# Performance work log

Measured on AMD Instinct MI355X. Metric: run time of the kernel, lower is better.

Reference implementation:

```python
import jax, jax.numpy as jnp
import numpy as np
import math

B, NQ, NK = 32, 1024, 1024
DQ = DK = DV = 512
H = 8
EPS = 1e-5


def _layernorm(x, g, b):
    mu = jnp.mean(x, axis=-1, keepdims=True)
    var = jnp.mean(jnp.square(x - mu), axis=-1, keepdims=True)
    return (x - mu) * jax.lax.rsqrt(var + EPS) * g + b


def setup_inputs() -> dict:
    key = jax.random.key(0)
    ks = jax.random.split(key, 8)
    s = 0.03  # small init scale for linear weights
    return {
        "Q": jax.random.normal(ks[0], (B, NQ, DQ), jnp.float32),
        "K": jax.random.normal(ks[1], (B, NK, DK), jnp.float32),
        "Wq": jax.random.normal(ks[2], (DQ, DV), jnp.float32) * s,
        "bq": jnp.zeros((DV,), jnp.float32),
        "Wk": jax.random.normal(ks[3], (DK, DV), jnp.float32) * s,
        "bk": jnp.zeros((DV,), jnp.float32),
        "Wv": jax.random.normal(ks[4], (DK, DV), jnp.float32) * s,
        "bv": jnp.zeros((DV,), jnp.float32),
        "Wo": jax.random.normal(ks[5], (DV, DV), jnp.float32) * s,
        "bo": jnp.zeros((DV,), jnp.float32),
        "g0": jnp.ones((DV,), jnp.float32),
        "beta0": jnp.zeros((DV,), jnp.float32),
        "g1": jnp.ones((DV,), jnp.float32),
        "beta1": jnp.zeros((DV,), jnp.float32),
    }


def reference(Q, K, Wq, bq, Wk, bk, Wv, bv, Wo, bo, g0, beta0, g1, beta1):
    b, nq, _ = Q.shape
    nk = K.shape[1]
    d = DV // H  # head dim (dim_split)

    q = Q @ Wq + bq            # [B, Nq, DV]
    k = K @ Wk + bk            # [B, Nk, DV]
    v = K @ Wv + bv            # [B, Nk, DV]

    # torch.cat(x.split(d, 2), 0) == reshape to [B,N,H,d] then stack heads on batch dim
    qh = q.reshape(b, nq, H, d).transpose(2, 0, 1, 3)  # [H, B, Nq, d]
    kh = k.reshape(b, nk, H, d).transpose(2, 0, 1, 3)  # [H, B, Nk, d]
    vh = v.reshape(b, nk, H, d).transpose(2, 0, 1, 3)  # [H, B, Nk, d]

    # NOTE: scaled by sqrt(dim_V), and softmax over the QUERY axis (torch dim=1)
    scores = jnp.einsum('hbqd,hbkd->hbqk', qh, kh) / math.sqrt(DV)
    A = jax.nn.softmax(scores, axis=2)                 # over Nq (faithful to source)
    oh = qh + jnp.einsum('hbqk,hbkd->hbqd', A, vh)     # residual on Q_

    out = oh.transpose(1, 2, 0, 3).reshape(b, nq, DV)  # merge heads back
    out = _layernorm(out, g0, beta0)
    out = out + jax.nn.relu(out @ Wo + bo)
    out = _layernorm(out, g1, beta1)
    return out
```

## Files before the change

kernel.cpp:

```cpp
#include <hip/hip_runtime.h>

#define Bz  32
#define NQz 1024
#define NKz 1024
#define SCALE 0.04419417382415922f

typedef __bf16 bf16_t;
typedef bf16_t bf16x8 __attribute__((ext_vector_type(8)));
typedef bf16_t bf16x4 __attribute__((ext_vector_type(4)));
typedef float  f32x4  __attribute__((ext_vector_type(4)));

#define MFMA16(a, b, c) __builtin_amdgcn_mfma_f32_16x16x32_bf16(a, b, c, 0, 0, 0)

__device__ __forceinline__ void gll16(const void* g, void* l) {
  __builtin_amdgcn_global_load_lds(
      (const __attribute__((address_space(1))) void*)g,
      (__attribute__((address_space(3))) void*)l, 16, 0, 0);
}

__device__ __forceinline__ bf16x8 cvt8(float4 a, float4 b) {
  bf16x8 r;
  r[0] = (bf16_t)a.x; r[1] = (bf16_t)a.y; r[2] = (bf16_t)a.z; r[3] = (bf16_t)a.w;
  r[4] = (bf16_t)b.x; r[5] = (bf16_t)b.y; r[6] = (bf16_t)b.z; r[7] = (bf16_t)b.w;
  return r;
}

__global__ void transpose_w(const float* __restrict__ W0, const float* __restrict__ W1,
                            const float* __restrict__ W2, const float* __restrict__ W3,
                            bf16_t* __restrict__ out) {
  __shared__ float tile[32][33];
  const float* W = blockIdx.z == 0 ? W0 : blockIdx.z == 1 ? W1 : blockIdx.z == 2 ? W2 : W3;
  bf16_t* o = out + (size_t)blockIdx.z * 512 * 512;
  const int n0 = blockIdx.x * 32, k0 = blockIdx.y * 32;
  const int tx = threadIdx.x, ty = threadIdx.y;
  for (int i = 0; i < 4; i++)
    tile[ty + i * 8][tx] = W[(size_t)(k0 + ty + i * 8) * 512 + n0 + tx];
  __syncthreads();
  for (int i = 0; i < 4; i++)
    o[(size_t)(n0 + ty + i * 8) * 512 + k0 + tx] = (bf16_t)tile[tx][ty + i * 8];
}

template <int DUAL>
__global__ __launch_bounds__(256) void gemm_f32a(const float* __restrict__ A,
                                                 const bf16_t* __restrict__ Wt,
                                                 const float* __restrict__ b0v,
                                                 const float* __restrict__ b1v,
                                                 float mult0,
                                                 bf16_t* __restrict__ C0,
                                                 bf16_t* __restrict__ C1) {
  __shared__ __align__(16) bf16_t As[128][40];
  __shared__ __align__(16) bf16_t Bs[128 * 32];
  const int t = threadIdx.x;
  const int wave = t >> 6, lane = t & 63;
  const int quad = lane >> 4, l16 = lane & 15;
  const int wm = wave & 1, wn = wave >> 1;
  const int m0 = blockIdx.x * 128, n0 = blockIdx.y * 128;
  const int r = t >> 1, half = t & 1;
  const int drow = lane >> 2;
  const int dg = (lane & 3) ^ ((lane >> 3) & 3);

  f32x4 acc[4][4] = {};

  for (int k0 = 0; k0 < 512; k0 += 32) {
    __syncthreads();
    for (int p = 0; p < 2; p++) {
      const bf16_t* src = Wt + (size_t)(n0 + p * 64 + wave * 16 + drow) * 512 + k0 + dg * 8;
      gll16(src, &Bs[(p * 256 + wave * 64) * 8]);
    }
    {
      const float* ap = A + (size_t)(m0 + r) * 512 + k0 + half * 16;
      float4 a0 = *(const float4*)(ap + 0);
      float4 a1 = *(const float4*)(ap + 4);
      float4 a2 = *(const float4*)(ap + 8);
      float4 a3 = *(const float4*)(ap + 12);
      *(bf16x8*)&As[r][half * 16 + 0] = cvt8(a0, a1);
      *(bf16x8*)&As[r][half * 16 + 8] = cvt8(a2, a3);
    }
    __syncthreads();
    bf16x8 af[4], bfv[4];
    for (int mt = 0; mt < 4; mt++)
      af[mt] = *(const bf16x8*)&As[wm * 64 + mt * 16 + l16][quad * 8];
    for (int nt = 0; nt < 4; nt++) {
      const int rB = wn * 64 + nt * 16 + l16;
      bfv[nt] = *(const bf16x8*)&Bs[rB * 32 + ((quad ^ ((rB >> 1) & 3)) * 8)];
    }
    for (int mt = 0; mt < 4; mt++)
      for (int nt = 0; nt < 4; nt++)
        acc[mt][nt] = MFMA16(af[mt], bfv[nt], acc[mt][nt]);
  }

  const float* bias = (!DUAL || n0 < 512) ? b0v : b1v;
  bf16_t* C = (!DUAL || n0 < 512) ? C0 : C1;
  const float mult = (!DUAL || n0 < 512) ? mult0 : 1.0f;
  const int nb = (!DUAL || n0 < 512) ? n0 : n0 - 512;
  for (int mt = 0; mt < 4; mt++) {
    for (int nt = 0; nt < 4; nt++) {
      const int row = m0 + wm * 64 + mt * 16 + quad * 4;
      const int col = nb + wn * 64 + nt * 16 + l16;
      const float bv = bias[col];
      for (int rg = 0; rg < 4; rg++)
        C[(size_t)(row + rg) * 512 + col] = (bf16_t)((acc[mt][nt][rg] + bv) * mult);
    }
  }
}

__global__ __launch_bounds__(256) void gemm_bf16a(const bf16_t* __restrict__ A,
                                                  const bf16_t* __restrict__ Wt,
                                                  const float* __restrict__ bias,
                                                  bf16_t* __restrict__ C) {
  __shared__ __align__(16) bf16_t As[128][40];
  __shared__ __align__(16) bf16_t Bs[128 * 32];
  const int t = threadIdx.x;
  const int wave = t >> 6, lane = t & 63;
  const int quad = lane >> 4, l16 = lane & 15;
  const int wm = wave & 1, wn = wave >> 1;
  const int m0 = blockIdx.x * 128, n0 = blockIdx.y * 128;
  const int r = t >> 1, half = t & 1;
  const int drow = lane >> 2;
  const int dg = (lane & 3) ^ ((lane >> 3) & 3);

  f32x4 acc[4][4] = {};

  for (int k0 = 0; k0 < 512; k0 += 32) {
    __syncthreads();
    for (int p = 0; p < 2; p++) {
      const bf16_t* src = Wt + (size_t)(n0 + p * 64 + wave * 16 + drow) * 512 + k0 + dg * 8;
      gll16(src, &Bs[(p * 256 + wave * 64) * 8]);
    }
    {
      const bf16_t* ap = A + (size_t)(m0 + r) * 512 + k0 + half * 16;
      *(bf16x8*)&As[r][half * 16 + 0] = *(const bf16x8*)(ap + 0);
      *(bf16x8*)&As[r][half * 16 + 8] = *(const bf16x8*)(ap + 8);
    }
    __syncthreads();
    bf16x8 af[4], bfv[4];
    for (int mt = 0; mt < 4; mt++)
      af[mt] = *(const bf16x8*)&As[wm * 64 + mt * 16 + l16][quad * 8];
    for (int nt = 0; nt < 4; nt++) {
      const int rB = wn * 64 + nt * 16 + l16;
      bfv[nt] = *(const bf16x8*)&Bs[rB * 32 + ((quad ^ ((rB >> 1) & 3)) * 8)];
    }
    for (int mt = 0; mt < 4; mt++)
      for (int nt = 0; nt < 4; nt++)
        acc[mt][nt] = MFMA16(af[mt], bfv[nt], acc[mt][nt]);
  }

  for (int mt = 0; mt < 4; mt++) {
    for (int nt = 0; nt < 4; nt++) {
      const int row = m0 + wm * 64 + mt * 16 + quad * 4;
      const int col = n0 + wn * 64 + nt * 16 + l16;
      const float bv = bias[col];
      for (int rg = 0; rg < 4; rg++) {
        float v = acc[mt][nt][rg] + bv;
        float x = (float)A[(size_t)(row + rg) * 512 + col];
        C[(size_t)(row + rg) * 512 + col] = (bf16_t)(x + fmaxf(v, 0.f));
      }
    }
  }
}

__global__ __launch_bounds__(256) void attn_stats(const bf16_t* __restrict__ qp,
                                                  const bf16_t* __restrict__ kp,
                                                  const bf16_t* __restrict__ vp,
                                                  bf16_t* __restrict__ Vt) {
  __shared__ __align__(16) bf16_t Vs[256 * 64];
  __shared__ __align__(16) bf16_t Qs[64 * 64];
  __shared__ float ls[256];
  const int t = threadIdx.x;
  const int wave = t >> 6, lane = t & 63;
  const int quad = lane >> 4, l16 = lane & 15;
  const int id = blockIdx.x;
  const int kb = ((id >> 3) & 3) * 256;
  const int hb = (id & 7) * 32 + (id >> 5);
  const int h = hb >> 5, b = hb & 31;
  const bf16_t* qbase = qp + (size_t)b * NQz * 512 + h * 64;
  const bf16_t* kbase = kp + (size_t)b * NKz * 512 + h * 64;
  const bf16_t* vbase = vp + (size_t)b * NKz * 512 + h * 64;
  const int drow = lane >> 3;
  const int dg = (lane & 7) ^ drow;

  for (int p = 0; p < 8; p++) {
    const bf16_t* src = vbase + (size_t)(kb + wave * 64 + p * 8 + (lane >> 3)) * 512 + (lane & 7) * 8;
    gll16(src, &Vs[(wave * 64 + p * 8) * 64]);
  }

  bf16x8 aK[4][2];
  for (int mt = 0; mt < 4; mt++) {
    const bf16_t* kr = kbase + (size_t)(kb + wave * 64 + mt * 16 + l16) * 512 + quad * 8;
    aK[mt][0] = *(const bf16x8*)kr;
    aK[mt][1] = *(const bf16x8*)(kr + 32);
  }

  f32x4 lacc[4] = {};
  for (int q0 = 0; q0 < NQz; q0 += 64) {
    __syncthreads();
    for (int p = 0; p < 2; p++) {
      const bf16_t* src = qbase + (size_t)(q0 + p * 32 + wave * 8 + drow) * 512 + dg * 8;
      gll16(src, &Qs[(p * 256 + wave * 64) * 8]);
    }
    __syncthreads();
    for (int nt = 0; nt < 4; nt++) {
      const int rQ = nt * 16 + l16;
      bf16x8 b0 = *(const bf16x8*)&Qs[rQ * 64 + ((quad ^ (rQ & 7)) * 8)];
      bf16x8 b1 = *(const bf16x8*)&Qs[rQ * 64 + (((quad + 4) ^ (rQ & 7)) * 8)];
      for (int mt = 0; mt < 4; mt++) {
        f32x4 s = {0.f, 0.f, 0.f, 0.f};
        s = MFMA16(aK[mt][0], b0, s);
        s = MFMA16(aK[mt][1], b1, s);
        lacc[mt][0] += __expf(s[0]);
        lacc[mt][1] += __expf(s[1]);
        lacc[mt][2] += __expf(s[2]);
        lacc[mt][3] += __expf(s[3]);
      }
    }
  }
  for (int mt = 0; mt < 4; mt++) {
    for (int rg = 0; rg < 4; rg++) {
      float v = lacc[mt][rg];
      v += __shfl_xor(v, 1);
      v += __shfl_xor(v, 2);
      v += __shfl_xor(v, 4);
      v += __shfl_xor(v, 8);
      if (l16 == 0) ls[wave * 64 + mt * 16 + quad * 4 + rg] = 1.0f / v;
    }
  }
  __syncthreads();
  const int d = t >> 2, kc = (t & 3) * 64;
  bf16_t* vtr = Vt + (size_t)hb * 64 * 1024 + (size_t)d * 1024 + kb + kc;
  for (int c = 0; c < 8; c++) {
    bf16x8 o;
    for (int j = 0; j < 8; j++)
      o[j] = (bf16_t)((float)Vs[(kc + c * 8 + j) * 64 + d] * ls[kc + c * 8 + j]);
    *(bf16x8*)(vtr + c * 8) = o;
  }
}

__global__ __launch_bounds__(256) void attn_out(const bf16_t* __restrict__ qp,
                                                const bf16_t* __restrict__ kp,
                                                const bf16_t* __restrict__ Vt,
                                                bf16_t* __restrict__ oh) {
  __shared__ __align__(16) bf16_t Ks[64 * 64];
  __shared__ __align__(16) bf16_t Vts[64 * 64];
  __shared__ __align__(16) bf16_t Ps[256][72];
  const int t = threadIdx.x;
  const int wave = t >> 6, lane = t & 63;
  const int quad = lane >> 4, l16 = lane & 15;
  const int id = blockIdx.x;
  const int qt = (id >> 3) & 3;
  const int hb = (id & 7) * 32 + (id >> 5);
  const int h = hb >> 5, b = hb & 31;
  const int q0 = qt * 256;
  const bf16_t* qbase = qp + (size_t)b * NQz * 512 + h * 64;
  const bf16_t* kbase = kp + (size_t)b * NKz * 512 + h * 64;
  const bf16_t* vtbase = Vt + (size_t)hb * 64 * 1024;
  const int drow = lane >> 3;
  const int dg = (lane & 7) ^ drow;

  bf16x8 bQ[4][2];
  for (int nt = 0; nt < 4; nt++) {
    const bf16_t* qr = qbase + (size_t)(q0 + wave * 64 + nt * 16 + l16) * 512 + quad * 8;
    bQ[nt][0] = *(const bf16x8*)qr;
    bQ[nt][1] = *(const bf16x8*)(qr + 32);
  }

  f32x4 acc[4][4] = {};
  for (int kk = 0; kk < NKz; kk += 64) {
    __syncthreads();
    for (int p = 0; p < 2; p++) {
      const bf16_t* ksrc = kbase + (size_t)(kk + p * 32 + wave * 8 + drow) * 512 + dg * 8;
      gll16(ksrc, &Ks[(p * 256 + wave * 64) * 8]);
      const bf16_t* vsrc = vtbase + (size_t)(p * 32 + wave * 8 + drow) * 1024 + kk + dg * 8;
      gll16(vsrc, &Vts[(p * 256 + wave * 64) * 8]);
    }
    __syncthreads();
    for (int mt = 0; mt < 4; mt++) {
      const int rK = mt * 16 + l16;
      bf16x8 a0 = *(const bf16x8*)&Ks[rK * 64 + ((quad ^ (rK & 7)) * 8)];
      bf16x8 a1 = *(const bf16x8*)&Ks[rK * 64 + (((quad + 4) ^ (rK & 7)) * 8)];
      for (int nt = 0; nt < 4; nt++) {
        f32x4 s = {0.f, 0.f, 0.f, 0.f};
        s = MFMA16(a0, bQ[nt][0], s);
        s = MFMA16(a1, bQ[nt][1], s);
        bf16x4 pk;
        pk[0] = (bf16_t)__expf(s[0]);
        pk[1] = (bf16_t)__expf(s[1]);
        pk[2] = (bf16_t)__expf(s[2]);
        pk[3] = (bf16_t)__expf(s[3]);
        *(bf16x4*)&Ps[wave * 64 + nt * 16 + l16][mt * 16 + quad * 4] = pk;
      }
    }
    bf16x8 aP[4][2];
    for (int mt = 0; mt < 4; mt++) {
      aP[mt][0] = *(const bf16x8*)&Ps[wave * 64 + mt * 16 + l16][quad * 8];
      aP[mt][1] = *(const bf16x8*)&Ps[wave * 64 + mt * 16 + l16][quad * 8 + 32];
    }
    for (int nd = 0; nd < 4; nd++) {
      const int rV = nd * 16 + l16;
      bf16x8 b0 = *(const bf16x8*)&Vts[rV * 64 + ((quad ^ (rV & 7)) * 8)];
      bf16x8 b1 = *(const bf16x8*)&Vts[rV * 64 + (((quad + 4) ^ (rV & 7)) * 8)];
      for (int mt = 0; mt < 4; mt++) {
        acc[mt][nd] = MFMA16(aP[mt][0], b0, acc[mt][nd]);
        acc[mt][nd] = MFMA16(aP[mt][1], b1, acc[mt][nd]);
      }
    }
  }
  for (int mt = 0; mt < 4; mt++)
    for (int nd = 0; nd < 4; nd++)
      for (int rg = 0; rg < 4; rg++)
        Ps[wave * 64 + mt * 16 + quad * 4 + rg][nd * 16 + l16] = (bf16_t)acc[mt][nd][rg];
  for (int rr = 0; rr < 2; rr++) {
    const int row = wave * 64 + rr * 32 + (lane >> 1), cc = (lane & 1) * 32;
    bf16_t* orow = oh + ((size_t)b * NQz + q0 + row) * 512 + h * 64 + cc;
    for (int c = 0; c < 4; c++)
      *(bf16x8*)(orow + c * 8) = *(const bf16x8*)&Ps[row][cc + c * 8];
  }
}

template <int RES, int F32OUT>
__global__ __launch_bounds__(256) void ln_k(const bf16_t* __restrict__ x,
                                            const bf16_t* __restrict__ res,
                                            const float* __restrict__ g,
                                            const float* __restrict__ be,
                                            bf16_t* __restrict__ yb,
                                            float* __restrict__ yf) {
  const int wave = threadIdx.x >> 6, lane = threadIdx.x & 63;
  const size_t row = (size_t)blockIdx.x * 4 + wave;
  bf16x8 xv = *(const bf16x8*)(x + row * 512 + lane * 8);
  float xf[8];
  for (int i = 0; i < 8; i++) xf[i] = (float)xv[i];
  if (RES) {
    bf16x8 rv = *(const bf16x8*)(res + row * 512 + lane * 8);
    for (int i = 0; i < 8; i++) xf[i] += (float)rv[i];
  }
  float s = 0.f, sq = 0.f;
  for (int i = 0; i < 8; i++) { s += xf[i]; sq += xf[i] * xf[i]; }
  for (int off = 1; off < 64; off <<= 1) {
    s += __shfl_xor(s, off);
    sq += __shfl_xor(sq, off);
  }
  const float mu = s * (1.0f / 512.0f);
  const float var = sq * (1.0f / 512.0f) - mu * mu;
  const float rstd = rsqrtf(var + 1e-5f);
  float4 gv0 = *(const float4*)(g + lane * 8);
  float4 gv1 = *(const float4*)(g + lane * 8 + 4);
  float4 bv0 = *(const float4*)(be + lane * 8);
  float4 bv1 = *(const float4*)(be + lane * 8 + 4);
  float gg[8] = {gv0.x, gv0.y, gv0.z, gv0.w, gv1.x, gv1.y, gv1.z, gv1.w};
  float bb[8] = {bv0.x, bv0.y, bv0.z, bv0.w, bv1.x, bv1.y, bv1.z, bv1.w};
  float o[8];
  for (int i = 0; i < 8; i++) o[i] = (xf[i] - mu) * rstd * gg[i] + bb[i];
  if (F32OUT) {
    float4 o0 = {o[0], o[1], o[2], o[3]}, o1 = {o[4], o[5], o[6], o[7]};
    *(float4*)(yf + row * 512 + lane * 8) = o0;
    *(float4*)(yf + row * 512 + lane * 8 + 4) = o1;
  } else {
    bf16x8 ov;
    for (int i = 0; i < 8; i++) ov[i] = (bf16_t)o[i];
    *(bf16x8*)(yb + row * 512 + lane * 8) = ov;
  }
}

extern "C" void kernel_launch(void* const* d_in, const int* in_sizes, int n_in,
                              void* d_out, int out_size, void* d_ws, size_t ws_size,
                              hipStream_t stream) {
  (void)in_sizes; (void)n_in; (void)out_size; (void)ws_size;
  const float* Q   = (const float*)d_in[0];
  const float* K   = (const float*)d_in[1];
  const float* Wq  = (const float*)d_in[2];
  const float* bq  = (const float*)d_in[3];
  const float* Wk  = (const float*)d_in[4];
  const float* bk  = (const float*)d_in[5];
  const float* Wv  = (const float*)d_in[6];
  const float* bv  = (const float*)d_in[7];
  const float* Wo  = (const float*)d_in[8];
  const float* bo  = (const float*)d_in[9];
  const float* g0  = (const float*)d_in[10];
  const float* be0 = (const float*)d_in[11];
  const float* g1  = (const float*)d_in[12];
  const float* be1 = (const float*)d_in[13];
  float* outp = (float*)d_out;

  char* w = (char*)d_ws;
  bf16_t* Wt  = (bf16_t*)w;
  bf16_t* qp  = (bf16_t*)(w + (2ull << 20));
  bf16_t* kp  = (bf16_t*)(w + (34ull << 20));
  bf16_t* vp  = (bf16_t*)(w + (66ull << 20));
  bf16_t* Vt  = (bf16_t*)(w + (98ull << 20));
  bf16_t* ohb = (bf16_t*)(w + (130ull << 20));
  bf16_t* x0b = vp;
  bf16_t* oh2 = kp;

  transpose_w<<<dim3(16, 16, 4), dim3(32, 8), 0, stream>>>(Wq, Wk, Wv, Wo, Wt);
  gemm_f32a<0><<<dim3(256, 4), 256, 0, stream>>>(Q, Wt, bq, nullptr, 1.0f, qp, nullptr);
  gemm_f32a<1><<<dim3(256, 8), 256, 0, stream>>>(K, Wt + (1 << 18), bk, bv, SCALE, kp, vp);
  attn_stats<<<1024, 256, 0, stream>>>(qp, kp, vp, Vt);
  attn_out<<<1024, 256, 0, stream>>>(qp, kp, Vt, ohb);
  ln_k<1, 0><<<8192, 256, 0, stream>>>(ohb, qp, g0, be0, x0b, nullptr);
  gemm_bf16a<<<dim3(256, 4), 256, 0, stream>>>(x0b, Wt + 3 * (1 << 18), bo, oh2);
  ln_k<0, 1><<<8192, 256, 0, stream>>>(oh2, nullptr, g1, be1, nullptr, outp);
}
```

Baseline: 494.8 us.

## Feed exp scores straight from registers into PV MFMA via transposed K16 layout

Rewrites the attention-output inner loop so the exponentiated score fragments stay in registers. They are used directly as the B operand of 16x16x16 bf16 MFMAs against V-transposed tiles, which makes the output transposed (d x q). This removes the Ps shared-memory staging buffer, its writes and reads, and the LDS round trip in the epilogue; output is now written directly from accumulators as 8-byte stores. The trade-off is twice as many MFMA instructions of half the K depth and narrower, less coalesced global stores.

```diff
diff --git a/kernel.cpp b/kernel.cpp
--- a/kernel.cpp
+++ b/kernel.cpp
@@ -9,8 +9,20 @@
 typedef bf16_t bf16x8 __attribute__((ext_vector_type(8)));
 typedef bf16_t bf16x4 __attribute__((ext_vector_type(4)));
 typedef float  f32x4  __attribute__((ext_vector_type(4)));
+typedef short  s16x4  __attribute__((ext_vector_type(4)));
 
 #define MFMA16(a, b, c) __builtin_amdgcn_mfma_f32_16x16x32_bf16(a, b, c, 0, 0, 0)
+
+__device__ __forceinline__ f32x4 mfma_k16(s16x4 a, s16x4 b, f32x4 c) {
+#if __has_builtin(__builtin_amdgcn_mfma_f32_16x16x16bf16_1k)
+  return __builtin_amdgcn_mfma_f32_16x16x16bf16_1k(a, b, c, 0, 0, 0);
+#else
+  f32x4 d;
+  asm volatile("v_mfma_f32_16x16x16_bf16 %0, %1, %2, %3"
+               : "=v"(d) : "v"(a), "v"(b), "v"(c));
+  return d;
+#endif
+}
 
 __device__ __forceinline__ void gll16(const void* g, void* l) {
   __builtin_amdgcn_global_load_lds(
@@ -241,7 +253,6 @@
                                                 bf16_t* __restrict__ oh) {
   __shared__ __align__(16) bf16_t Ks[64 * 64];
   __shared__ __align__(16) bf16_t Vts[64 * 64];
-  __shared__ __align__(16) bf16_t Ps[256][72];
   const int t = threadIdx.x;
   const int wave = t >> 6, lane = t & 63;
   const int quad = lane >> 4, l16 = lane & 15;
@@ -277,6 +288,13 @@
       const int rK = mt * 16 + l16;
       bf16x8 a0 = *(const bf16x8*)&Ks[rK * 64 + ((quad ^ (rK & 7)) * 8)];
       bf16x8 a1 = *(const bf16x8*)&Ks[rK * 64 + (((quad + 4) ^ (rK & 7)) * 8)];
+      s16x4 aV[4];
+      for (int nd = 0; nd < 4; nd++) {
+        const int rV = nd * 16 + l16;
+        const int g = 2 * mt + (quad >> 1);
+        const int off = ((g ^ (rV & 7)) << 3) + (quad & 1) * 4;
+        aV[nd] = *(const s16x4*)&Vts[rV * 64 + off];
+      }
       for (int nt = 0; nt < 4; nt++) {
         f32x4 s = {0.f, 0.f, 0.f, 0.f};
         s = MFMA16(a0, bQ[nt][0], s);
@@ -286,33 +304,20 @@
         pk[1] = (bf16_t)__expf(s[1]);
         pk[2] = (bf16_t)__expf(s[2]);
         pk[3] = (bf16_t)__expf(s[3]);
-        *(bf16x4*)&Ps[wave * 64 + nt * 16 + l16][mt * 16 + quad * 4] = pk;
+        const s16x4 bp = __builtin_bit_cast(s16x4, pk);
+        for (int nd = 0; nd < 4; nd++)
+          acc[nd][nt] = mfma_k16(aV[nd], bp, acc[nd][nt]);
       }
     }
-    bf16x8 aP[4][2];
-    for (int mt = 0; mt < 4; mt++) {
-      aP[mt][0] = *(const bf16x8*)&Ps[wave * 64 + mt * 16 + l16][quad * 8];
-      aP[mt][1] = *(const bf16x8*)&Ps[wave * 64 + mt * 16 + l16][quad * 8 + 32];
-    }
+  }
+  for (int nt = 0; nt < 4; nt++) {
+    const int q = q0 + wave * 64 + nt * 16 + l16;
+    bf16_t* orow = oh + ((size_t)b * NQz + q) * 512 + h * 64;
     for (int nd = 0; nd < 4; nd++) {
-      const int rV = nd * 16 + l16;
-      bf16x8 b0 = *(const bf16x8*)&Vts[rV * 64 + ((quad ^ (rV & 7)) * 8)];
-      bf16x8 b1 = *(const bf16x8*)&Vts[rV * 64 + (((quad + 4) ^ (rV & 7)) * 8)];
-      for (int mt = 0; mt < 4; mt++) {
-        acc[mt][nd] = MFMA16(aP[mt][0], b0, acc[mt][nd]);
-        acc[mt][nd] = MFMA16(aP[mt][1], b1, acc[mt][nd]);
-      }
-    }
-  }
-  for (int mt = 0; mt < 4; mt++)
-    for (int nd = 0; nd < 4; nd++)
-      for (int rg = 0; rg < 4; rg++)
-        Ps[wave * 64 + mt * 16 + quad * 4 + rg][nd * 16 + l16] = (bf16_t)acc[mt][nd][rg];
-  for (int rr = 0; rr < 2; rr++) {
-    const int row = wave * 64 + rr * 32 + (lane >> 1), cc = (lane & 1) * 32;
-    bf16_t* orow = oh + ((size_t)b * NQz + q0 + row) * 512 + h * 64 + cc;
-    for (int c = 0; c < 4; c++)
-      *(bf16x8*)(orow + c * 8) = *(const bf16x8*)&Ps[row][cc + c * 8];
+      bf16x4 ov;
+      for (int rg = 0; rg < 4; rg++) ov[rg] = (bf16_t)acc[nd][nt][rg];
+      *(bf16x4*)(orow + nd * 16 + quad * 4) = ov;
+    }
   }
 }
 
```

After: 533.9 us. 7.9% more time.
